# Optimization experiments

Measured on AMD Instinct MI355X. Metric: run time of the kernel, lower is better.

## Reference

```python
import jax, jax.numpy as jnp
import numpy as np

N_NODES = 100000
N_EDGES = 600000
VOCAB = 5000
NUM_GRAPHS = 2000
NUM_CLASSES = 10


def setup_inputs() -> dict:
    key = jax.random.key(0)
    ks = jax.random.split(key, 12)
    x = jax.random.randint(ks[0], (N_NODES,), 0, VOCAB, dtype=jnp.int32)
    edge_index = jax.random.randint(ks[1], (2, N_EDGES), 0, N_NODES, dtype=jnp.int32)
    batch = jnp.sort(jax.random.randint(ks[2], (N_NODES,), 0, NUM_GRAPHS, dtype=jnp.int32))
    emb = jax.random.normal(ks[3], (VOCAB, 64), dtype=jnp.float32) * 0.1
    W1 = jax.random.normal(ks[4], (64, 128), dtype=jnp.float32) * (1.0 / np.sqrt(64))
    b1 = jnp.zeros((128,), dtype=jnp.float32)
    W2 = jax.random.normal(ks[5], (128, 128), dtype=jnp.float32) * (1.0 / np.sqrt(128))
    b2 = jnp.zeros((128,), dtype=jnp.float32)
    Wlin = jax.random.normal(ks[6], (128, NUM_CLASSES), dtype=jnp.float32) * (1.0 / np.sqrt(128))
    blin = jnp.zeros((NUM_CLASSES,), dtype=jnp.float32)
    return {"x": x, "edge_index": edge_index, "batch": batch, "num_graphs": NUM_GRAPHS,
            "emb": emb, "W1": W1, "b1": b1, "W2": W2, "b2": b2, "Wlin": Wlin, "blin": blin}


def reference(x, edge_index, batch, num_graphs, emb, W1, b1, W2, b2, Wlin, blin):
    N = x.shape[0]
    loops = jnp.arange(N, dtype=edge_index.dtype)
    src = jnp.concatenate([edge_index[0], loops])  # message sources (j)
    dst = jnp.concatenate([edge_index[1], loops])  # aggregation targets (i)
    # GCN symmetric normalization with self-loops (PyG gcn_norm, source_to_target)
    deg = jax.ops.segment_sum(jnp.ones_like(dst, dtype=jnp.float32), dst, num_segments=N)
    dinv = jnp.where(deg > 0, jax.lax.rsqrt(deg), 0.0)
    norm = dinv[src] * dinv[dst]  # [E+N]

    def gcn(h, W, b):
        h = h @ W  # linear transform first (GCNConv order)
        msg = h[src] * norm[:, None]  # gather + scale, [E+N, F]
        return jax.ops.segment_sum(msg, dst, num_segments=N) + b

    h = emb[x]  # [N, 64]
    h = jax.nn.relu(gcn(h, W1, b1))
    h = jax.nn.relu(gcn(h, W2, b2))
    g = jax.ops.segment_max(h, batch, num_segments=num_graphs)  # global_max_pool
    return g @ Wlin + blin
```

## Files before the change

### kernel.cpp

```cpp
#include <hip/hip_runtime.h>
#include <hip/hip_bf16.h>
#include <hip/hip_fp16.h>


typedef _Float16 h8 __attribute__((ext_vector_type(8)));
typedef _Float16 h4v __attribute__((ext_vector_type(4)));
typedef float f32x4 __attribute__((ext_vector_type(4)));

__global__ __launch_bounds__(256) void k_zero(int4* __restrict__ deg, int n4i,
                                              int4* __restrict__ pool, int p4i) {
    int t = blockIdx.x * 256 + threadIdx.x;
    int4 z = make_int4(0, 0, 0, 0);
    if (t < n4i) deg[t] = z;
    if (t < p4i) pool[t] = z;
}

__global__ __launch_bounds__(256) void k_degprep(const int* __restrict__ dst, int* __restrict__ deg, int E,
                                                 const float* __restrict__ emb, __half2* __restrict__ e16,
                                                 const float* __restrict__ W1, _Float16* __restrict__ W1T,
                                                 const float* __restrict__ W2, _Float16* __restrict__ W2T,
                                                 int nEmbF, int gE, int nCast) {
    int bid = blockIdx.x;
    if (bid < gE) {
        int e = bid * 256 + threadIdx.x;
        if (e < E) atomicAdd(&deg[dst[e]], 1);
    } else if (bid < gE + nCast) {
        int t = (bid - gE) * 256 + threadIdx.x;
        if (t * 4 < nEmbF) {
            float4 v = *(const float4*)&emb[t * 4];
            e16[t * 2] = __floats2half2_rn(v.x, v.y);
            e16[t * 2 + 1] = __floats2half2_rn(v.z, v.w);
        }
    } else if (bid < gE + nCast + 32) {
        int t = (bid - gE - nCast) * 256 + threadIdx.x;
        int c = t >> 6, k = t & 63;
        W1T[c * 64 + k] = (_Float16)W1[k * 128 + c];
    } else {
        int t = (bid - gE - nCast - 32) * 256 + threadIdx.x;
        if (t < 128 * 128) {
            int c = t >> 7, k = t & 127;
            W2T[c * 128 + k] = (_Float16)W2[k * 128 + c];
        }
    }
}

__global__ __launch_bounds__(256) void k_scan1(const int* __restrict__ deg, int* __restrict__ exc,
                                               int* __restrict__ bsums, float* __restrict__ dinv, int N) {
    __shared__ int s[256];
    int i = blockIdx.x * 256 + threadIdx.x;
    int v = (i < N) ? deg[i] : 0;
    if (i < N) dinv[i] = rsqrtf((float)(v + 1));
    s[threadIdx.x] = v;
    __syncthreads();
    for (int off = 1; off < 256; off <<= 1) {
        int t = (threadIdx.x >= (unsigned)off) ? s[threadIdx.x - off] : 0;
        __syncthreads();
        s[threadIdx.x] += t;
        __syncthreads();
    }
    if (i < N) exc[i] = s[threadIdx.x] - v;
    if (threadIdx.x == 255) bsums[blockIdx.x] = s[255];
}

__global__ __launch_bounds__(512) void k_scan2(int* __restrict__ bsums, int nb) {
    __shared__ int s[512];
    int i = threadIdx.x;
    int v = (i < nb) ? bsums[i] : 0;
    s[i] = v;
    __syncthreads();
    for (int off = 1; off < 512; off <<= 1) {
        int t = (i >= off) ? s[i - off] : 0;
        __syncthreads();
        s[i] += t;
        __syncthreads();
    }
    if (i < nb) bsums[i] = s[i] - v;
}

__global__ __launch_bounds__(256) void k_scan3(int* __restrict__ rowstart, int* __restrict__ cursor,
                                               const int* __restrict__ bsums, int N, int E) {
    int i = blockIdx.x * 256 + threadIdx.x;
    if (i < N) {
        int r = rowstart[i] + bsums[blockIdx.x];
        rowstart[i] = r;
        cursor[i] = r;
    }
    if (i == 0 && blockIdx.x == 0) rowstart[N] = E;
}

__global__ __launch_bounds__(256) void k_fill(const int* __restrict__ src, const int* __restrict__ dst,
                                              const int* __restrict__ x, const float* __restrict__ dinv,
                                              int* __restrict__ cursor, int2* __restrict__ ed,
                                              int* __restrict__ cols, int E) {
    int e = blockIdx.x * 256 + threadIdx.x;
    if (e < E) {
        int d = dst[e];
        int s = src[e];
        int pos = atomicAdd(&cursor[d], 1);
        ed[pos] = make_int2(x[s], __float_as_int(dinv[s]));
        cols[pos] = s;
    }
}

__global__ __launch_bounds__(256) void k_mlp(const __half2* __restrict__ e16, const int* __restrict__ x,
                                             const float* __restrict__ dinv, const int* __restrict__ rs,
                                             const int2* __restrict__ ed, const _Float16* __restrict__ W1T,
                                             const float* __restrict__ b1, const _Float16* __restrict__ W2T,
                                             _Float16* __restrict__ P, int N) {
    __shared__ _Float16 Xs[64][72];
    __shared__ _Float16 Hs[64][136];
    int tid = threadIdx.x;
    int blk0 = blockIdx.x * 64;
    {
        int lane = tid & 31;
        int hw = tid >> 5;
        for (int pass = 0; pass < 4; ++pass) {
            int nl = hw * 8 + pass * 2;
            int gA = blk0 + nl;     if (gA >= N) gA = N - 1;
            int gB = blk0 + nl + 1; if (gB >= N) gB = N - 1;
            int cA0 = rs[gA], cA1 = rs[gA + 1];
            int cB0 = rs[gB], cB1 = rs[gB + 1];
            bool hasA = cA0 < cA1, hasB = cB0 < cB1;
            __half2 tA[8], tB[8];
            float wA[8], wB[8];
#pragma unroll
            for (int i = 0; i < 8; ++i) {
                int ei = cA0 + i;
                int ec = (ei < cA1) ? ei : (hasA ? cA1 - 1 : 0);
                int2 r2 = ed[ec];
                tA[i] = e16[(size_t)r2.x * 32 + lane];
                wA[i] = (ei < cA1) ? __int_as_float(r2.y) : 0.f;
            }
#pragma unroll
            for (int i = 0; i < 8; ++i) {
                int ei = cB0 + i;
                int ec = (ei < cB1) ? ei : (hasB ? cB1 - 1 : 0);
                int2 r2 = ed[ec];
                tB[i] = e16[(size_t)r2.x * 32 + lane];
                wB[i] = (ei < cB1) ? __int_as_float(r2.y) : 0.f;
            }
            float dA = dinv[gA], dB = dinv[gB];
            float2 sA = __half22float2(e16[(size_t)x[gA] * 32 + lane]);
            float2 sB = __half22float2(e16[(size_t)x[gB] * 32 + lane]);
            float aA0 = dA * sA.x, aA1 = dA * sA.y;
            float aB0 = dB * sB.x, aB1 = dB * sB.y;
#pragma unroll
            for (int i = 0; i < 8; ++i) {
                float2 tf = __half22float2(tA[i]);
                aA0 = fmaf(wA[i], tf.x, aA0);
                aA1 = fmaf(wA[i], tf.y, aA1);
            }
#pragma unroll
            for (int i = 0; i < 8; ++i) {
                float2 tf = __half22float2(tB[i]);
                aB0 = fmaf(wB[i], tf.x, aB0);
                aB1 = fmaf(wB[i], tf.y, aB1);
            }
            for (int e = cA0 + 8; e < cA1; e += 8) {
#pragma unroll
                for (int i = 0; i < 8; ++i) {
                    int ei = e + i;
                    int ec = (ei < cA1) ? ei : cA1 - 1;
                    int2 r2 = ed[ec];
                    tA[i] = e16[(size_t)r2.x * 32 + lane];
                    wA[i] = (ei < cA1) ? __int_as_float(r2.y) : 0.f;
                }
#pragma unroll
                for (int i = 0; i < 8; ++i) {
                    float2 tf = __half22float2(tA[i]);
                    aA0 = fmaf(wA[i], tf.x, aA0);
                    aA1 = fmaf(wA[i], tf.y, aA1);
                }
            }
            for (int e = cB0 + 8; e < cB1; e += 8) {
#pragma unroll
                for (int i = 0; i < 8; ++i) {
                    int ei = e + i;
                    int ec = (ei < cB1) ? ei : cB1 - 1;
                    int2 r2 = ed[ec];
                    tB[i] = e16[(size_t)r2.x * 32 + lane];
                    wB[i] = (ei < cB1) ? __int_as_float(r2.y) : 0.f;
                }
#pragma unroll
                for (int i = 0; i < 8; ++i) {
                    float2 tf = __half22float2(tB[i]);
                    aB0 = fmaf(wB[i], tf.x, aB0);
                    aB1 = fmaf(wB[i], tf.y, aB1);
                }
            }
            *(__half2*)&Xs[nl][lane * 2] = __floats2half2_rn(dA * aA0, dA * aA1);
            *(__half2*)&Xs[nl + 1][lane * 2] = __floats2half2_rn(dB * aB0, dB * aB1);
        }
    }
    __syncthreads();
    int l = tid & 63, wid = tid >> 6;
    int r = l & 15, kg = l >> 4;
    {
        f32x4 acc[8];
#pragma unroll
        for (int ct = 0; ct < 8; ++ct) acc[ct] = (f32x4){0.f, 0.f, 0.f, 0.f};
#pragma unroll
        for (int kc = 0; kc < 2; ++kc) {
            h8 a = *(const h8*)&Xs[wid * 16 + r][kc * 32 + kg * 8];
#pragma unroll
            for (int ct = 0; ct < 8; ++ct) {
                h8 b = *(const h8*)(W1T + (size_t)r * 64 + kg * 8 + kc * 32 + ct * 1024);
                acc[ct] = __builtin_amdgcn_mfma_f32_16x16x32_f16(a, b, acc[ct], 0, 0, 0);
            }
        }
#pragma unroll
        for (int ct = 0; ct < 8; ++ct) {
            float bias = b1[ct * 16 + r];
#pragma unroll
            for (int i = 0; i < 4; ++i)
                Hs[wid * 16 + 4 * kg + i][ct * 16 + r] = (_Float16)fmaxf(acc[ct][i] + bias, 0.f);
        }
    }
    __syncthreads();
    {
        f32x4 acc[8];
#pragma unroll
        for (int ct = 0; ct < 8; ++ct) acc[ct] = (f32x4){0.f, 0.f, 0.f, 0.f};
#pragma unroll
        for (int kc = 0; kc < 4; ++kc) {
            h8 a = *(const h8*)&Hs[wid * 16 + r][kc * 32 + kg * 8];
#pragma unroll
            for (int ct = 0; ct < 8; ++ct) {
                h8 b = *(const h8*)(W2T + (size_t)r * 128 + kg * 8 + kc * 32 + ct * 2048);
                acc[ct] = __builtin_amdgcn_mfma_f32_16x16x32_f16(a, b, acc[ct], 0, 0, 0);
            }
        }
        float dv[4];
#pragma unroll
        for (int i = 0; i < 4; ++i) {
            int gr = blk0 + wid * 16 + 4 * kg + i;
            dv[i] = (gr < N) ? dinv[gr] : 0.f;
        }
#pragma unroll
        for (int ct = 0; ct < 8; ++ct) {
#pragma unroll
            for (int i = 0; i < 4; ++i) {
                int gr = blk0 + wid * 16 + 4 * kg + i;
                if (gr < N) P[(size_t)gr * 128 + ct * 16 + r] = (_Float16)(acc[ct][i] * dv[i]);
            }
        }
    }
}

__global__ __launch_bounds__(256) void k_agg2pool(const h4v* __restrict__ P4, const int* __restrict__ batch,
                                                  const float* __restrict__ dinv, const int* __restrict__ rs,
                                                  const int* __restrict__ cols, const float4* __restrict__ bias4,
                                                  float* __restrict__ pool, int N, int G) {
    __shared__ int lpool[4][128];
    int tid = threadIdx.x;
    lpool[tid >> 7][tid & 127] = 0;
    lpool[(tid >> 7) + 2][tid & 127] = 0;
    __syncthreads();
    int lane = tid & 31;
    int blk_n0 = blockIdx.x * 16;
    int gfirst = batch[(blk_n0 < N) ? blk_n0 : (N - 1)];
    int n0 = blk_n0 + (tid >> 5) * 2;
    if (n0 < N) {
        int nA = n0;
        int nB = (n0 + 1 < N) ? n0 + 1 : n0;
        int cA0 = rs[nA], cA1 = rs[nA + 1];
        int cB0 = rs[nB], cB1 = rs[nB + 1];
        bool hasA = cA0 < cA1, hasB = cB0 < cB1;
        h4v sA = P4[(size_t)nA * 32 + lane];
        h4v sB = P4[(size_t)nB * 32 + lane];
        float aA[4], aB[4];
#pragma unroll
        for (int f = 0; f < 4; ++f) {
            aA[f] = (float)sA[f];
            aB[f] = (float)sB[f];
        }
        {
            h4v tA[16], tB[16];
#pragma unroll
            for (int i = 0; i < 16; ++i) {
                int ei = cA0 + i;
                int ec = (ei < cA1) ? ei : (hasA ? cA1 - 1 : 0);
                tA[i] = P4[(size_t)cols[ec] * 32 + lane];
            }
#pragma unroll
            for (int i = 0; i < 16; ++i) {
                int ei = cB0 + i;
                int ec = (ei < cB1) ? ei : (hasB ? cB1 - 1 : 0);
                tB[i] = P4[(size_t)cols[ec] * 32 + lane];
            }
#pragma unroll
            for (int i = 0; i < 16; ++i) {
                float w = (cA0 + i < cA1) ? 1.f : 0.f;
#pragma unroll
                for (int f = 0; f < 4; ++f) aA[f] = fmaf(w, (float)tA[i][f], aA[f]);
            }
#pragma unroll
            for (int i = 0; i < 16; ++i) {
                float w = (cB0 + i < cB1) ? 1.f : 0.f;
#pragma unroll
                for (int f = 0; f < 4; ++f) aB[f] = fmaf(w, (float)tB[i][f], aB[f]);
            }
        }
        for (int e = cA0 + 16; e < cA1; e += 16) {
            h4v t[16];
#pragma unroll
            for (int i = 0; i < 16; ++i) {
                int ei = e + i;
                int ec = (ei < cA1) ? ei : cA1 - 1;
                t[i] = P4[(size_t)cols[ec] * 32 + lane];
            }
#pragma unroll
            for (int i = 0; i < 16; ++i) {
                float w = (e + i < cA1) ? 1.f : 0.f;
#pragma unroll
                for (int f = 0; f < 4; ++f) aA[f] = fmaf(w, (float)t[i][f], aA[f]);
            }
        }
        for (int e = cB0 + 16; e < cB1; e += 16) {
            h4v t[16];
#pragma unroll
            for (int i = 0; i < 16; ++i) {
                int ei = e + i;
                int ec = (ei < cB1) ? ei : cB1 - 1;
                t[i] = P4[(size_t)cols[ec] * 32 + lane];
            }
#pragma unroll
            for (int i = 0; i < 16; ++i) {
                float w = (e + i < cB1) ? 1.f : 0.f;
#pragma unroll
                for (int f = 0; f < 4; ++f) aB[f] = fmaf(w, (float)t[i][f], aB[f]);
            }
        }
        float dA = dinv[nA], dB = dinv[nB];
        int gA = batch[nA], gB = batch[nB];
        float4 b = bias4[lane];
        float bv[4] = {b.x, b.y, b.z, b.w};
        float zA[4], zB[4];
#pragma unroll
        for (int f = 0; f < 4; ++f) {
            zA[f] = fmaxf(fmaf(dA, aA[f], bv[f]), 0.f);
            zB[f] = fmaxf(fmaf(dB, aB[f], bv[f]), 0.f);
        }
        int rot = (lane >> 3) & 3;
        auto emit = [&](int g, const float* m) {
            int slot = g - gfirst;
            if (slot < 4) {
#pragma unroll
                for (int f = 0; f < 4; ++f) {
                    int ff = (f + rot) & 3;
                    if (m[ff] > 0.f) atomicMax(&lpool[slot][lane * 4 + ff], __float_as_int(m[ff]));
                }
            } else {
                float* pg = pool + (size_t)g * 128 + lane * 4;
#pragma unroll
                for (int f = 0; f < 4; ++f)
                    if (m[f] > 0.f) atomicMax((int*)(pg + f), __float_as_int(m[f]));
            }
        };
        if (gA == gB) {
            float m[4];
#pragma unroll
            for (int f = 0; f < 4; ++f) m[f] = fmaxf(zA[f], zB[f]);
            emit(gA, m);
        } else {
            emit(gA, zA);
            emit(gB, zB);
        }
    }
    __syncthreads();
    {
        int f = tid & 127;
        for (int s = tid >> 7; s < 4; s += 2) {
            int v = lpool[s][f];
            if (v > 0) atomicMax((int*)&pool[(size_t)(gfirst + s) * 128 + f], v);
        }
    }
}

__global__ __launch_bounds__(256) void k_final(const float* __restrict__ pool, const float* __restrict__ Wlin,
                                               const float* __restrict__ blin, float* __restrict__ out, int G) {
    int t = blockIdx.x * 256 + threadIdx.x;
    if (t >= G * 10) return;
    int g = t / 10, c = t % 10;
    float acc = blin[c];
    const float* pr = pool + (size_t)g * 128;
#pragma unroll 8
    for (int f = 0; f < 128; ++f) acc = fmaf(pr[f], Wlin[f * 10 + c], acc);
    out[t] = acc;
}

extern "C" void kernel_launch(void* const* d_in, const int* in_sizes, int n_in,
                              void* d_out, int out_size, void* d_ws, size_t ws_size,
                              hipStream_t stream) {
    const int* x = (const int*)d_in[0];
    const int* ei = (const int*)d_in[1];
    const int* batch = (const int*)d_in[2];
    const float* emb = (const float*)d_in[4];
    const float* W1 = (const float*)d_in[5];
    const float* b1 = (const float*)d_in[6];
    const float* W2 = (const float*)d_in[7];
    const float* b2 = (const float*)d_in[8];
    const float* Wlin = (const float*)d_in[9];
    const float* blin = (const float*)d_in[10];
    float* out = (float*)d_out;

    int N = in_sizes[0];
    int E = in_sizes[1] / 2;
    int VOCAB = in_sizes[4] / 64;
    int G = out_size / 10;
    const int* srcp = ei;
    const int* dstp = ei + E;

    char* p = (char*)d_ws;
    auto alloc = [&](size_t bytes) -> char* {
        char* r = p;
        p += (bytes + 255) & ~(size_t)255;
        return r;
    };
    int* deg = (int*)alloc((size_t)N * 4);
    int* cursor = (int*)alloc((size_t)N * 4);
    int* rowstart = (int*)alloc((size_t)(N + 1) * 4);
    int* bsums = (int*)alloc(512 * 4);
    float* dinv = (float*)alloc((size_t)N * 4);
    int2* ed = (int2*)alloc((size_t)E * 8);
    int* cols = (int*)alloc((size_t)E * 4);
    _Float16* e16 = (_Float16*)alloc((size_t)VOCAB * 64 * 2);
    _Float16* W1T = (_Float16*)alloc(128 * 64 * 2);
    _Float16* W2T = (_Float16*)alloc(128 * 128 * 2);
    _Float16* P = (_Float16*)alloc((size_t)N * 128 * 2);
    float* pool = (float*)alloc((size_t)G * 128 * 4);

    int gE = (E + 255) / 256;
    int gN = (N + 255) / 256;
    int nEmbF = VOCAB * 64;
    int nCast = (nEmbF / 4 + 255) / 256;

    int n4i = N / 4, p4i = G * 128 / 4;
    int zg = ((n4i > p4i ? n4i : p4i) + 255) / 256;
    k_zero<<<zg, 256, 0, stream>>>((int4*)deg, n4i, (int4*)pool, p4i);
    k_degprep<<<gE + nCast + 32 + 64, 256, 0, stream>>>(dstp, deg, E, emb, (__half2*)e16, W1, W1T,
                                                        W2, W2T, nEmbF, gE, nCast);
    k_scan1<<<gN, 256, 0, stream>>>(deg, rowstart, bsums, dinv, N);
    k_scan2<<<1, 512, 0, stream>>>(bsums, gN);
    k_scan3<<<gN, 256, 0, stream>>>(rowstart, cursor, bsums, N, E);
    k_fill<<<gE, 256, 0, stream>>>(srcp, dstp, x, dinv, cursor, ed, cols, E);
    k_mlp<<<(N + 63) / 64, 256, 0, stream>>>((const __half2*)e16, x, dinv, rowstart, ed, W1T, b1,
                                             W2T, P, N);
    k_agg2pool<<<(N + 15) / 16, 256, 0, stream>>>((const h4v*)P, batch, dinv, rowstart, cols,
                                                  (const float4*)b2, pool, N, G);
    k_final<<<(G * 10 + 255) / 256, 256, 0, stream>>>(pool, Wlin, blin, out, G);
}
```

Before: 196.5 us.

## Split fused aggregate+MLP kernel into separate gather and GEMM kernels

The first-layer neighbour aggregation moves out of k_mlp into its own kernel, k_agge. Each half-wave in it handles two nodes and writes the fp16 aggregated features to a padded global buffer Xagg. A new k_gemm12 then reads Xagg directly for the two MFMA layers. The aim is to spread the irregular gather over many more small blocks and decouple it from the GEMM's occupancy and shared-memory limits. The per-edge int2 record and the separate cols array are merged into one 16-byte int4 record. The change costs an extra global write and read of the aggregated features, an extra launch, and wider edge records that k_agg2pool now reads only to get the column index.

Result: no change. 197.6 us (+0.6%).

```diff
diff --git a/kernel.cpp b/kernel.cpp
--- a/kernel.cpp
+++ b/kernel.cpp
@@ -7,12 +7,14 @@
 typedef _Float16 h4v __attribute__((ext_vector_type(4)));
 typedef float f32x4 __attribute__((ext_vector_type(4)));
 
-__global__ __launch_bounds__(256) void k_zero(int4* __restrict__ deg, int n4i,
-                                              int4* __restrict__ pool, int p4i) {
+__global__ __launch_bounds__(256) void k_zero(int4* __restrict__ deg4, int n4i,
+                                              int4* __restrict__ pool4, int p4i,
+                                              int4* __restrict__ xpad, int x4i) {
     int t = blockIdx.x * 256 + threadIdx.x;
     int4 z = make_int4(0, 0, 0, 0);
-    if (t < n4i) deg[t] = z;
-    if (t < p4i) pool[t] = z;
+    if (t < n4i) deg4[t] = z;
+    if (t < p4i) pool4[t] = z;
+    if (t < x4i) xpad[t] = z;
 }
 
 __global__ __launch_bounds__(256) void k_degprep(const int* __restrict__ dst, int* __restrict__ deg, int E,
@@ -90,121 +92,117 @@
 
 __global__ __launch_bounds__(256) void k_fill(const int* __restrict__ src, const int* __restrict__ dst,
                                               const int* __restrict__ x, const float* __restrict__ dinv,
-                                              int* __restrict__ cursor, int2* __restrict__ ed,
-                                              int* __restrict__ cols, int E) {
+                                              int* __restrict__ cursor, int4* __restrict__ rec, int E) {
     int e = blockIdx.x * 256 + threadIdx.x;
     if (e < E) {
         int d = dst[e];
         int s = src[e];
         int pos = atomicAdd(&cursor[d], 1);
-        ed[pos] = make_int2(x[s], __float_as_int(dinv[s]));
-        cols[pos] = s;
-    }
-}
-
-__global__ __launch_bounds__(256) void k_mlp(const __half2* __restrict__ e16, const int* __restrict__ x,
-                                             const float* __restrict__ dinv, const int* __restrict__ rs,
-                                             const int2* __restrict__ ed, const _Float16* __restrict__ W1T,
-                                             const float* __restrict__ b1, const _Float16* __restrict__ W2T,
-                                             _Float16* __restrict__ P, int N) {
-    __shared__ _Float16 Xs[64][72];
+        rec[pos] = make_int4(x[s], __float_as_int(dinv[s]), s, 0);
+    }
+}
+
+__global__ __launch_bounds__(256) void k_agge(const __half2* __restrict__ e16, const int* __restrict__ x,
+                                              const float* __restrict__ dinv, const int* __restrict__ rs,
+                                              const int4* __restrict__ rec, __half2* __restrict__ Xagg, int N) {
+    int lane = threadIdx.x & 31;
+    int n0 = (blockIdx.x * 8 + (threadIdx.x >> 5)) * 2;
+    if (n0 >= N) return;
+    int nB = (n0 + 1 < N) ? n0 + 1 : n0;
+    int cA0 = rs[n0], cA1 = rs[n0 + 1];
+    int cB0 = rs[nB], cB1 = rs[nB + 1];
+    bool hasA = cA0 < cA1, hasB = cB0 < cB1;
+    __half2 tA[8], tB[8];
+    float wA[8], wB[8];
+#pragma unroll
+    for (int i = 0; i < 8; ++i) {
+        int ei = cA0 + i;
+        int ec = (ei < cA1) ? ei : (hasA ? cA1 - 1 : 0);
+        int4 r2 = rec[ec];
+        tA[i] = e16[(size_t)r2.x * 32 + lane];
+        wA[i] = (ei < cA1) ? __int_as_float(r2.y) : 0.f;
+    }
+#pragma unroll
+    for (int i = 0; i < 8; ++i) {
+        int ei = cB0 + i;
+        int ec = (ei < cB1) ? ei : (hasB ? cB1 - 1 : 0);
+        int4 r2 = rec[ec];
+        tB[i] = e16[(size_t)r2.x * 32 + lane];
+        wB[i] = (ei < cB1) ? __int_as_float(r2.y) : 0.f;
+    }
+    float dA = dinv[n0], dB = dinv[nB];
+    float2 sA = __half22float2(e16[(size_t)x[n0] * 32 + lane]);
+    float2 sB = __half22float2(e16[(size_t)x[nB] * 32 + lane]);
+    float aA0 = dA * sA.x, aA1 = dA * sA.y;
+    float aB0 = dB * sB.x, aB1 = dB * sB.y;
+#pragma unroll
+    for (int i = 0; i < 8; ++i) {
+        float2 tf = __half22float2(tA[i]);
+        aA0 = fmaf(wA[i], tf.x, aA0);
+        aA1 = fmaf(wA[i], tf.y, aA1);
+    }
+#pragma unroll
+    for (int i = 0; i < 8; ++i) {
+        float2 tf = __half22float2(tB[i]);
+        aB0 = fmaf(wB[i], tf.x, aB0);
+        aB1 = fmaf(wB[i], tf.y, aB1);
+    }
+    for (int e = cA0 + 8; e < cA1; e += 8) {
+#pragma unroll
+        for (int i = 0; i < 8; ++i) {
+            int ei = e + i;
+            int ec = (ei < cA1) ? ei : cA1 - 1;
+            int4 r2 = rec[ec];
+            tA[i] = e16[(size_t)r2.x * 32 + lane];
+            wA[i] = (ei < cA1) ? __int_as_float(r2.y) : 0.f;
+        }
+#pragma unroll
+        for (int i = 0; i < 8; ++i) {
+            float2 tf = __half22float2(tA[i]);
+            aA0 = fmaf(wA[i], tf.x, aA0);
+            aA1 = fmaf(wA[i], tf.y, aA1);
+        }
+    }
+    for (int e = cB0 + 8; e < cB1; e += 8) {
+#pragma unroll
+        for (int i = 0; i < 8; ++i) {
+            int ei = e + i;
+            int ec = (ei < cB1) ? ei : cB1 - 1;
+            int4 r2 = rec[ec];
+            tB[i] = e16[(size_t)r2.x * 32 + lane];
+            wB[i] = (ei < cB1) ? __int_as_float(r2.y) : 0.f;
+        }
+#pragma unroll
+        for (int i = 0; i < 8; ++i) {
+            float2 tf = __half22float2(tB[i]);
+            aB0 = fmaf(wB[i], tf.x, aB0);
+            aB1 = fmaf(wB[i], tf.y, aB1);
+        }
+    }
+    Xagg[(size_t)n0 * 32 + lane] = __floats2half2_rn(dA * aA0, dA * aA1);
+    Xagg[(size_t)nB * 32 + lane] = __floats2half2_rn(dB * aB0, dB * aB1);
+}
+
+__global__ __launch_bounds__(256) void k_gemm12(const _Float16* __restrict__ Xagg,
+                                                const _Float16* __restrict__ W1T, const float* __restrict__ b1,
+                                                const _Float16* __restrict__ W2T, const float* __restrict__ dinv,
+                                                _Float16* __restrict__ P, int N) {
     __shared__ _Float16 Hs[64][136];
     int tid = threadIdx.x;
+    int l = tid & 63, wid = tid >> 6;
+    int r = l & 15, kg = l >> 4;
     int blk0 = blockIdx.x * 64;
     {
-        int lane = tid & 31;
-        int hw = tid >> 5;
-        for (int pass = 0; pass < 4; ++pass) {
-            int nl = hw * 8 + pass * 2;
-            int gA = blk0 + nl;     if (gA >= N) gA = N - 1;
-            int gB = blk0 + nl + 1; if (gB >= N) gB = N - 1;
-            int cA0 = rs[gA], cA1 = rs[gA + 1];
-            int cB0 = rs[gB], cB1 = rs[gB + 1];
-            bool hasA = cA0 < cA1, hasB = cB0 < cB1;
-            __half2 tA[8], tB[8];
-            float wA[8], wB[8];
-#pragma unroll
-            for (int i = 0; i < 8; ++i) {
-                int ei = cA0 + i;
-                int ec = (ei < cA1) ? ei : (hasA ? cA1 - 1 : 0);
-                int2 r2 = ed[ec];
-                tA[i] = e16[(size_t)r2.x * 32 + lane];
-                wA[i] = (ei < cA1) ? __int_as_float(r2.y) : 0.f;
-            }
-#pragma unroll
-            for (int i = 0; i < 8; ++i) {
-                int ei = cB0 + i;
-                int ec = (ei < cB1) ? ei : (hasB ? cB1 - 1 : 0);
-                int2 r2 = ed[ec];
-                tB[i] = e16[(size_t)r2.x * 32 + lane];
-                wB[i] = (ei < cB1) ? __int_as_float(r2.y) : 0.f;
-            }
-            float dA = dinv[gA], dB = dinv[gB];
-            float2 sA = __half22float2(e16[(size_t)x[gA] * 32 + lane]);
-            float2 sB = __half22float2(e16[(size_t)x[gB] * 32 + lane]);
-            float aA0 = dA * sA.x, aA1 = dA * sA.y;
-            float aB0 = dB * sB.x, aB1 = dB * sB.y;
-#pragma unroll
-            for (int i = 0; i < 8; ++i) {
-                float2 tf = __half22float2(tA[i]);
-                aA0 = fmaf(wA[i], tf.x, aA0);
-                aA1 = fmaf(wA[i], tf.y, aA1);
-            }
-#pragma unroll
-            for (int i = 0; i < 8; ++i) {
-                float2 tf = __half22float2(tB[i]);
-                aB0 = fmaf(wB[i], tf.x, aB0);
-                aB1 = fmaf(wB[i], tf.y, aB1);
-            }
-            for (int e = cA0 + 8; e < cA1; e += 8) {
-#pragma unroll
-                for (int i = 0; i < 8; ++i) {
-                    int ei = e + i;
-                    int ec = (ei < cA1) ? ei : cA1 - 1;
-                    int2 r2 = ed[ec];
-                    tA[i] = e16[(size_t)r2.x * 32 + lane];
-                    wA[i] = (ei < cA1) ? __int_as_float(r2.y) : 0.f;
-                }
-#pragma unroll
-                for (int i = 0; i < 8; ++i) {
-                    float2 tf = __half22float2(tA[i]);
-                    aA0 = fmaf(wA[i], tf.x, aA0);
-                    aA1 = fmaf(wA[i], tf.y, aA1);
-                }
-            }
-            for (int e = cB0 + 8; e < cB1; e += 8) {
-#pragma unroll
-                for (int i = 0; i < 8; ++i) {
-                    int ei = e + i;
-                    int ec = (ei < cB1) ? ei : cB1 - 1;
-                    int2 r2 = ed[ec];
-                    tB[i] = e16[(size_t)r2.x * 32 + lane];
-                    wB[i] = (ei < cB1) ? __int_as_float(r2.y) : 0.f;
-                }
-#pragma unroll
-                for (int i = 0; i < 8; ++i) {
-                    float2 tf = __half22float2(tB[i]);
-                    aB0 = fmaf(wB[i], tf.x, aB0);
-                    aB1 = fmaf(wB[i], tf.y, aB1);
-                }
-            }
-            *(__half2*)&Xs[nl][lane * 2] = __floats2half2_rn(dA * aA0, dA * aA1);
-            *(__half2*)&Xs[nl + 1][lane * 2] = __floats2half2_rn(dB * aB0, dB * aB1);
-        }
-    }
-    __syncthreads();
-    int l = tid & 63, wid = tid >> 6;
-    int r = l & 15, kg = l >> 4;
-    {
         f32x4 acc[8];
 #pragma unroll
         for (int ct = 0; ct < 8; ++ct) acc[ct] = (f32x4){0.f, 0.f, 0.f, 0.f};
+        const _Float16* ab = Xagg + (size_t)(blk0 + wid * 16 + r) * 64 + kg * 8;
 #pragma unroll
         for (int kc = 0; kc < 2; ++kc) {
-            h8 a = *(const h8*)&Xs[wid * 16 + r][kc * 32 + kg * 8];
+            h8 a = *(const h8*)(ab + kc * 32);
 #pragma unroll
             for (int ct = 0; ct < 8; ++ct) {
-                h8 b = *(const h8*)(W1T + (size_t)r * 64 + kg * 8 + kc * 32 + ct * 1024);
+                h8 b = *(const h8*)(W1T + (size_t)(ct * 16 + r) * 64 + kc * 32 + kg * 8);
                 acc[ct] = __builtin_amdgcn_mfma_f32_16x16x32_f16(a, b, acc[ct], 0, 0, 0);
             }
         }
@@ -226,7 +224,7 @@
             h8 a = *(const h8*)&Hs[wid * 16 + r][kc * 32 + kg * 8];
 #pragma unroll
             for (int ct = 0; ct < 8; ++ct) {
-                h8 b = *(const h8*)(W2T + (size_t)r * 128 + kg * 8 + kc * 32 + ct * 2048);
+                h8 b = *(const h8*)(W2T + (size_t)(ct * 16 + r) * 128 + kc * 32 + kg * 8);
                 acc[ct] = __builtin_amdgcn_mfma_f32_16x16x32_f16(a, b, acc[ct], 0, 0, 0);
             }
         }
@@ -249,7 +247,7 @@
 
 __global__ __launch_bounds__(256) void k_agg2pool(const h4v* __restrict__ P4, const int* __restrict__ batch,
                                                   const float* __restrict__ dinv, const int* __restrict__ rs,
-                                                  const int* __restrict__ cols, const float4* __restrict__ bias4,
+                                                  const int4* __restrict__ rec, const float4* __restrict__ bias4,
                                                   float* __restrict__ pool, int N, int G) {
     __shared__ int lpool[4][128];
     int tid = threadIdx.x;
@@ -280,13 +278,13 @@
             for (int i = 0; i < 16; ++i) {
                 int ei = cA0 + i;
                 int ec = (ei < cA1) ? ei : (hasA ? cA1 - 1 : 0);
-                tA[i] = P4[(size_t)cols[ec] * 32 + lane];
+                tA[i] = P4[(size_t)rec[ec].z * 32 + lane];
             }
 #pragma unroll
             for (int i = 0; i < 16; ++i) {
                 int ei = cB0 + i;
                 int ec = (ei < cB1) ? ei : (hasB ? cB1 - 1 : 0);
-                tB[i] = P4[(size_t)cols[ec] * 32 + lane];
+                tB[i] = P4[(size_t)rec[ec].z * 32 + lane];
             }
 #pragma unroll
             for (int i = 0; i < 16; ++i) {
@@ -307,7 +305,7 @@
             for (int i = 0; i < 16; ++i) {
                 int ei = e + i;
                 int ec = (ei < cA1) ? ei : cA1 - 1;
-                t[i] = P4[(size_t)cols[ec] * 32 + lane];
+                t[i] = P4[(size_t)rec[ec].z * 32 + lane];
             }
 #pragma unroll
             for (int i = 0; i < 16; ++i) {
@@ -322,7 +320,7 @@
             for (int i = 0; i < 16; ++i) {
                 int ei = e + i;
                 int ec = (ei < cB1) ? ei : cB1 - 1;
-                t[i] = P4[(size_t)cols[ec] * 32 + lane];
+                t[i] = P4[(size_t)rec[ec].z * 32 + lane];
             }
 #pragma unroll
             for (int i = 0; i < 16; ++i) {
@@ -417,16 +415,17 @@
         p += (bytes + 255) & ~(size_t)255;
         return r;
     };
+    int Npad = (N + 63) & ~63;
     int* deg = (int*)alloc((size_t)N * 4);
     int* cursor = (int*)alloc((size_t)N * 4);
     int* rowstart = (int*)alloc((size_t)(N + 1) * 4);
     int* bsums = (int*)alloc(512 * 4);
     float* dinv = (float*)alloc((size_t)N * 4);
-    int2* ed = (int2*)alloc((size_t)E * 8);
-    int* cols = (int*)alloc((size_t)E * 4);
+    int4* rec = (int4*)alloc((size_t)E * 16);
     _Float16* e16 = (_Float16*)alloc((size_t)VOCAB * 64 * 2);
     _Float16* W1T = (_Float16*)alloc(128 * 64 * 2);
     _Float16* W2T = (_Float16*)alloc(128 * 128 * 2);
+    _Float16* Xagg = (_Float16*)alloc((size_t)Npad * 64 * 2);
     _Float16* P = (_Float16*)alloc((size_t)N * 128 * 2);
     float* pool = (float*)alloc((size_t)G * 128 * 4);
 
@@ -436,17 +435,20 @@
     int nCast = (nEmbF / 4 + 255) / 256;
 
     int n4i = N / 4, p4i = G * 128 / 4;
-    int zg = ((n4i > p4i ? n4i : p4i) + 255) / 256;
-    k_zero<<<zg, 256, 0, stream>>>((int4*)deg, n4i, (int4*)pool, p4i);
+    int x4i = (Npad - N) * 64 * 2 / 16;
+    int zmax = n4i > p4i ? n4i : p4i;
+    k_zero<<<(zmax + 255) / 256, 256, 0, stream>>>((int4*)deg, n4i, (int4*)pool, p4i,
+                                                   (int4*)(Xagg + (size_t)N * 64), x4i);
     k_degprep<<<gE + nCast + 32 + 64, 256, 0, stream>>>(dstp, deg, E, emb, (__half2*)e16, W1, W1T,
                                                         W2, W2T, nEmbF, gE, nCast);
     k_scan1<<<gN, 256, 0, stream>>>(deg, rowstart, bsums, dinv, N);
     k_scan2<<<1, 512, 0, stream>>>(bsums, gN);
     k_scan3<<<gN, 256, 0, stream>>>(rowstart, cursor, bsums, N, E);
-    k_fill<<<gE, 256, 0, stream>>>(srcp, dstp, x, dinv, cursor, ed, cols, E);
-    k_mlp<<<(N + 63) / 64, 256, 0, stream>>>((const __half2*)e16, x, dinv, rowstart, ed, W1T, b1,
-                                             W2T, P, N);
-    k_agg2pool<<<(N + 15) / 16, 256, 0, stream>>>((const h4v*)P, batch, dinv, rowstart, cols,
+    k_fill<<<gE, 256, 0, stream>>>(srcp, dstp, x, dinv, cursor, rec, E);
+    k_agge<<<(N + 15) / 16, 256, 0, stream>>>((const __half2*)e16, x, dinv, rowstart, rec,
+                                              (__half2*)Xagg, N);
+    k_gemm12<<<(N + 63) / 64, 256, 0, stream>>>(Xagg, W1T, b1, W2T, dinv, P, N);
+    k_agg2pool<<<(N + 15) / 16, 256, 0, stream>>>((const h4v*)P, batch, dinv, rowstart, rec,
                                                   (const float4*)b2, pool, N, G);
     k_final<<<(G * 10 + 255) / 256, 256, 0, stream>>>(pool, Wlin, blin, out, G);
 }
```
